# Optimization experiments

Measured on AMD Instinct MI355X. Metric: run time of the kernel, lower is better.

## Reference

```python
import jax, jax.numpy as jnp
import numpy as np

GAMMA = 0.99
LMBD = 0.95  # lambda is unused in live math: in-loop advantages are overwritten by returns - values
EPS = 0.2
T, S, H, A = 262144, 128, 1024, 16


def setup_inputs() -> dict:
    key = jax.random.key(0)
    ks = jax.random.split(key, 12)
    states = jax.random.normal(ks[0], (T, S), jnp.float32)
    actions = jax.random.normal(ks[1], (T, A), jnp.float32)
    rewards = jax.random.normal(ks[2], (T, 1), jnp.float32)
    values = jax.random.normal(ks[3], (T, 1), jnp.float32)
    masks = jax.random.randint(ks[4], (T, 1), 0, 2, jnp.int32)
    W1 = jax.random.normal(ks[5], (S, H), jnp.float32) / np.sqrt(S)
    b1 = jnp.zeros((H,), jnp.float32)
    W_mu = jax.random.normal(ks[6], (H, A), jnp.float32) / np.sqrt(H)
    b_mu = jnp.zeros((A,), jnp.float32)
    W_lv = jax.random.normal(ks[7], (H, A), jnp.float32) / np.sqrt(H)
    b_lv = jnp.zeros((A,), jnp.float32)
    # beta (old policy) log-probs: computed from the same net + small noise so that
    # ratio = exp(sum(pi_logp - beta_logp)) stays numerically reasonable, as in real PPO.
    h = jnp.tanh(states @ W1 + b1)
    mu = h @ W_mu + b_mu
    std = jnp.exp(0.5 * (h @ W_lv + b_lv))
    logp = -0.5 * jnp.square((actions - mu) / std) - jnp.log(std) - 0.5 * jnp.log(2.0 * jnp.pi)
    beta_log_probs = logp + 0.01 * jax.random.normal(ks[8], (T, A), jnp.float32)
    return dict(states=states, actions=actions, rewards=rewards, values=values,
                beta_log_probs=beta_log_probs, W1=W1, b1=b1, W_mu=W_mu, b_mu=b_mu,
                W_lv=W_lv, b_lv=b_lv, masks=masks)


def reference(states, actions, rewards, values, beta_log_probs,
              W1, b1, W_mu, b_mu, W_lv, b_lv, masks):
    m = masks.astype(rewards.dtype)  # [T,1] 1=continue, 0=episode boundary

    # reversed masked discounted-return recurrence: returns[i] = r[i] + gamma * prev_return * m[i]
    def step(prev_ret, inp):
        r, mi = inp
        ret = r + GAMMA * prev_ret * mi
        return ret, ret

    _, returns = jax.lax.scan(step, jnp.zeros((1,), rewards.dtype), (rewards, m), reverse=True)
    # (deltas / in-loop GAE advantages in the source are dead code: overwritten below)
    advantages = returns - values                      # [T,1]
    a_hat = (advantages - advantages.mean()) / (advantages.std(ddof=1) + 1e-7)

    # pi(states) -> mu, logvar (value head unused here)
    h = jnp.tanh(states @ W1 + b1)                     # [T,H]
    mu = h @ W_mu + b_mu                               # [T,A]
    logvar = h @ W_lv + b_lv
    std = jnp.exp(0.5 * logvar)
    pi_log_probs = -0.5 * jnp.square((actions - mu) / std) - jnp.log(std) - 0.5 * jnp.log(2.0 * jnp.pi)

    blp = jax.lax.stop_gradient(beta_log_probs)        # .detach() in source
    ratio = jnp.exp(jnp.sum(pi_log_probs - blp, axis=1, keepdims=True))  # [T,1]

    actor_loss = -jnp.mean(jnp.minimum(ratio * a_hat,
                                       jnp.clip(ratio, 1.0 - EPS, 1.0 + EPS) * a_hat))
    critic_loss = jnp.mean(jnp.square(advantages))
    return actor_loss + critic_loss
```

## Files before the change

### kernel.cpp

```cpp
#include <hip/hip_runtime.h>
#include <math.h>


typedef __attribute__((ext_vector_type(8))) short short8_t;
typedef __attribute__((ext_vector_type(4))) short short4_t;
typedef __attribute__((ext_vector_type(4))) float float4_t;
typedef __attribute__((ext_vector_type(2))) unsigned uint2_t;
typedef __attribute__((ext_vector_type(4))) unsigned uint4_t;

#define T_TOTAL 262144
#define S_DIM 128
#define H_DIM 1024
#define A_DIM 16
#define GAMMA 0.99f
#define LOG2E2 2.8853900817779268f
#define SEG_LEN 64
#define NSEG 4096
#define GRP 16
#define NGRP 256

#define WS_SUM   0
#define WS_SUMSQ 1
#define WS_TERM  4
#define WS_SEGA  8
#define WS_SEGB  (WS_SEGA + NSEG)
#define WS_INC   (WS_SEGB + NSEG)
#define WS_ADV   (WS_INC + NSEG)
#define WS_W1F   (WS_ADV + T_TOTAL)
#define WS_WHF   (WS_W1F + 65536)
#define WS_B1S   (WS_WHF + 16384)

#define SM_SIZE 16400

__device__ __forceinline__ short f2bf(float f) {
  unsigned u = __float_as_uint(f);
  u += 0x7fffu + ((u >> 16) & 1u);
  return (short)(u >> 16);
}

__device__ __forceinline__ unsigned cvt_pk_bf16(float lo, float hi) {
  unsigned r;
  asm("v_cvt_pk_bf16_f32 %0, %1, %2" : "=v"(r) : "v"(lo), "v"(hi));
  return r;
}

__device__ __forceinline__ void permlane32_swap2(unsigned& a, unsigned& b) {
  asm("v_permlane32_swap_b32 %0, %1" : "+v"(a), "+v"(b));
}

__device__ __forceinline__ float tanh2(float x, float bs) {
  float a = __builtin_fmaf(x, LOG2E2, bs);
  float e = __builtin_amdgcn_exp2f(a);
  float r = __builtin_amdgcn_rcpf(e + 1.0f);
  return __builtin_fmaf(r, -2.0f, 1.0f);
}

__global__ void prep_all(const float* __restrict__ W1,
                         const float* __restrict__ W_mu,
                         const float* __restrict__ W_lv,
                         const float* __restrict__ b1,
                         const float* __restrict__ rewards,
                         const int* __restrict__ masks,
                         float* __restrict__ ws,
                         short* __restrict__ w1f,
                         short* __restrict__ whf) {
  const int blk = blockIdx.x;
  if (blk < 64) {
    int id = blk * 256 + threadIdx.x;
    int lane = id & 63;
    int kf = (id >> 6) & 3;
    int nt = id >> 8;
    int quad = lane >> 4, col = nt * 16 + (lane & 15);
    int kbase = kf * 32 + quad * 8;
#pragma unroll
    for (int e = 0; e < 8; ++e)
      w1f[(size_t)id * 8 + e] = f2bf(W1[(size_t)(kbase + e) * H_DIM + col]);
  } else if (blk < 80) {
    int id = (blk - 64) * 256 + threadIdx.x;
    int lane = id & 63;
    int kf = (id >> 6) & 31;
    int nt = id >> 11;
    const float* src = nt ? W_lv : W_mu;
    int quad = lane >> 4, col = lane & 15;
    int hbase = kf * 32 + ((quad >> 1) << 4) + ((quad & 1) << 2);
#pragma unroll
    for (int e = 0; e < 8; ++e) {
      int hh = hbase + ((e >> 2) << 3) + (e & 3);
      whf[(size_t)id * 8 + e] = f2bf(src[(size_t)hh * A_DIM + col]);
    }
  } else if (blk < 96) {
    int g = (blk - 80) * 256 + threadIdx.x;
    int lo = g * SEG_LEN;
    const float4* r4 = (const float4*)(rewards + lo);
    const int4* m4 = (const int4*)(masks + lo);
    float a = 1.0f, b = 0.0f;
#pragma unroll 4
    for (int c = 15; c >= 0; --c) {
      float4 r = r4[c]; int4 mm = m4[c];
      float gi;
      gi = GAMMA * (float)mm.w; b = r.w + gi * b; a = gi * a;
      gi = GAMMA * (float)mm.z; b = r.z + gi * b; a = gi * a;
      gi = GAMMA * (float)mm.y; b = r.y + gi * b; a = gi * a;
      gi = GAMMA * (float)mm.x; b = r.x + gi * b; a = gi * a;
    }
    ws[WS_SEGA + g] = a;
    ws[WS_SEGB + g] = b;
  } else {
    if (threadIdx.x < 8) ws[threadIdx.x] = 0.0f;
    int base = threadIdx.x * 4;
    float4 bv = *(const float4*)(b1 + base);
    float4 o;
    o.x = LOG2E2 * bv.x; o.y = LOG2E2 * bv.y;
    o.z = LOG2E2 * bv.z; o.w = LOG2E2 * bv.w;
    *(float4*)(ws + WS_B1S + base) = o;
  }
}

__global__ void scan_pass2(float* __restrict__ ws) {
  __shared__ float gA[NGRP], gB[NGRP], ginc[NGRP];
  int t = threadIdx.x;
  int lo = t * GRP, hi = lo + GRP - 1;
  float A = 1.0f, B = 0.0f;
  for (int s = hi; s >= lo; --s) {
    float as = ws[WS_SEGA + s], bs = ws[WS_SEGB + s];
    B = bs + as * B;
    A = as * A;
  }
  gA[t] = A; gB[t] = B;
  __syncthreads();
  if (t == 0) {
    float x = 0.0f;
    ginc[NGRP - 1] = 0.0f;
    for (int g = NGRP - 1; g >= 1; --g) {
      x = gB[g] + gA[g] * x;
      ginc[g - 1] = x;
    }
  }
  __syncthreads();
  float x = ginc[t];
  for (int s = hi; s >= lo; --s) {
    ws[WS_INC + s] = x;
    x = ws[WS_SEGB + s] + ws[WS_SEGA + s] * x;
  }
}

__global__ void scan_pass3(const float* __restrict__ rewards,
                           const int* __restrict__ masks,
                           const float* __restrict__ values,
                           float* __restrict__ ws) {
  int g = blockIdx.x * blockDim.x + threadIdx.x;
  int lo = g * SEG_LEN;
  float x = ws[WS_INC + g];
  const float4* r4 = (const float4*)(rewards + lo);
  const int4* m4 = (const int4*)(masks + lo);
  const float4* v4 = (const float4*)(values + lo);
  float4* adv4 = (float4*)(ws + WS_ADV + lo);
  float s1 = 0.0f, s2 = 0.0f;
#pragma unroll 4
  for (int c = 15; c >= 0; --c) {
    float4 r = r4[c]; int4 mm = m4[c]; float4 v = v4[c];
    float gi;
    gi = GAMMA * (float)mm.w; x = r.w + gi * x; float aw = x - v.w;
    gi = GAMMA * (float)mm.z; x = r.z + gi * x; float az = x - v.z;
    gi = GAMMA * (float)mm.y; x = r.y + gi * x; float ay = x - v.y;
    gi = GAMMA * (float)mm.x; x = r.x + gi * x; float ax = x - v.x;
    float4 o; o.x = ax; o.y = ay; o.z = az; o.w = aw;
    adv4[c] = o;
    s1 += ax + ay + az + aw;
    s2 += ax * ax + ay * ay + az * az + aw * aw;
  }
  for (int m = 1; m < 64; m <<= 1) {
    s1 += __shfl_xor(s1, m);
    s2 += __shfl_xor(s2, m);
  }
  if ((threadIdx.x & 63) == 0) {
    atomicAdd(&ws[WS_SUM], s1);
    atomicAdd(&ws[WS_SUMSQ], s2);
  }
}

__launch_bounds__(256, 2)
__global__ void main2(const float* __restrict__ states,
                      const float* __restrict__ actions,
                      const float* __restrict__ beta,
                      const float* __restrict__ b1s,
                      const float* __restrict__ bmug,
                      const float* __restrict__ blvg,
                      const short* __restrict__ W1f,
                      const short* __restrict__ Whf,
                      float* __restrict__ ws) {
  __shared__ __align__(16) unsigned char smem[SM_SIZE];
  short* Ab = (short*)smem;

  const int tid = threadIdx.x;
  const int lane = tid & 63;
  const int w = tid >> 6;
  const int quad = lane >> 4;
  const int t0 = blockIdx.x * 64;

  {
    const float4* src = (const float4*)(states + (size_t)t0 * S_DIM);
#pragma unroll
    for (int i = 0; i < 8; ++i) {
      int f = tid + i * 256;
      float4 v = src[f];
      int row = f >> 5, kq = f & 31;
      int rt = row >> 4, rr = row & 15;
      int k = kq * 4, kf = k >> 5, qd = (k >> 3) & 3, j0 = k & 7;
      uint2_t pk2;
      pk2[0] = cvt_pk_bf16(v.x, v.y);
      pk2[1] = cvt_pk_bf16(v.z, v.w);
      *(uint2_t*)(Ab + (((rt * 4 + kf) * 64 + qd * 16 + rr) << 3) + j0) = pk2;
    }
  }
  __syncthreads();

  short8_t sfrag[4][4];
#pragma unroll
  for (int rt = 0; rt < 4; ++rt)
#pragma unroll
    for (int kf = 0; kf < 4; ++kf)
      sfrag[rt][kf] = *((const short8_t*)Ab + (rt * 4 + kf) * 64 + lane);

  float4_t acc2[4][2];
#pragma unroll
  for (int rt = 0; rt < 4; ++rt) {
    acc2[rt][0] = (float4_t){0.f, 0.f, 0.f, 0.f};
    acc2[rt][1] = (float4_t){0.f, 0.f, 0.f, 0.f};
  }
  const float4_t zz = (float4_t){0.f, 0.f, 0.f, 0.f};

  for (int kk = 0; kk < 8; ++kk) {
    const int nt1 = w * 16 + kk * 2;
    const short8_t* w1p = (const short8_t*)W1f + nt1 * 256 + lane;
    short8_t wf0[4], wf1[4];
#pragma unroll
    for (int kf = 0; kf < 4; ++kf) {
      wf0[kf] = w1p[kf * 64];
      wf1[kf] = w1p[256 + kf * 64];
    }
    const float4 b1a = *(const float4*)(b1s + nt1 * 16 + quad * 4);
    const float4 b1b = *(const float4*)(b1s + nt1 * 16 + 16 + quad * 4);
    const int kf2 = w * 8 + kk;
    const short8_t* whp = (const short8_t*)Whf + kf2 * 64 + lane;
    const short8_t wmu = whp[0];
    const short8_t wlv = whp[2048];
#pragma unroll
    for (int rt = 0; rt < 4; ++rt) {
      float4_t c0 = zz;
      float4_t c1 = zz;
#pragma unroll
      for (int kf = 0; kf < 4; ++kf) {
        c0 = __builtin_amdgcn_mfma_f32_16x16x32_bf16(wf0[kf], sfrag[rt][kf], c0, 0, 0, 0);
        c1 = __builtin_amdgcn_mfma_f32_16x16x32_bf16(wf1[kf], sfrag[rt][kf], c1, 0, 0, 0);
      }
      unsigned p00 = cvt_pk_bf16(tanh2(c0[0], b1a.x), tanh2(c0[1], b1a.y));
      unsigned p01 = cvt_pk_bf16(tanh2(c0[2], b1a.z), tanh2(c0[3], b1a.w));
      unsigned p10 = cvt_pk_bf16(tanh2(c1[0], b1b.x), tanh2(c1[1], b1b.y));
      unsigned p11 = cvt_pk_bf16(tanh2(c1[2], b1b.z), tanh2(c1[3], b1b.w));
      permlane32_swap2(p00, p10);
      permlane32_swap2(p01, p11);
      uint4_t u = (uint4_t){p00, p01, p10, p11};
      short8_t b2 = __builtin_bit_cast(short8_t, u);
      acc2[rt][0] = __builtin_amdgcn_mfma_f32_16x16x32_bf16(wmu, b2, acc2[rt][0], 0, 0, 0);
      acc2[rt][1] = __builtin_amdgcn_mfma_f32_16x16x32_bf16(wlv, b2, acc2[rt][1], 0, 0, 0);
    }
  }

  __syncthreads();
  float* red = (float*)smem;
  float* lds_term = (float*)(smem + 16384);
  if (w < 2) {
#pragma unroll
    for (int rt = 0; rt < 4; ++rt)
#pragma unroll
      for (int nt = 0; nt < 2; ++nt)
        *(float4_t*)(red + ((((w & 1) * 8 + rt * 2 + nt) * 64 + lane) << 2)) = acc2[rt][nt];
  }
  __syncthreads();
  if (w >= 2) {
#pragma unroll
    for (int rt = 0; rt < 4; ++rt)
#pragma unroll
      for (int nt = 0; nt < 2; ++nt) {
        float* p = red + ((((w & 1) * 8 + rt * 2 + nt) * 64 + lane) << 2);
        float4_t v = *(float4_t*)p;
        v += acc2[rt][nt];
        *(float4_t*)p = v;
      }
  }
  __syncthreads();

  const float s1 = ws[WS_SUM], s2 = ws[WS_SUMSQ];
  const float n = (float)T_TOTAL;
  const float mean = s1 / n;
  float var = (s2 - s1 * s1 / n) / (n - 1.0f);
  var = fmaxf(var, 0.0f);
  const float istd = 1.0f / (sqrtf(var) + 1e-7f);

  const int rt = w;
  const int tcol = lane & 15;
  const int t = t0 + rt * 16 + tcol;
  const float4 bmu4 = *(const float4*)(bmug + quad * 4);
  const float4 blv4 = *(const float4*)(blvg + quad * 4);
  float m0 = bmu4.x, m1 = bmu4.y, m2 = bmu4.z, m3 = bmu4.w;
  float l0 = blv4.x, l1 = blv4.y, l2 = blv4.z, l3 = blv4.w;
  const float4_t* rp = (const float4_t*)red;
#pragma unroll
  for (int r = 0; r < 2; ++r) {
    float4_t mv = rp[(r * 8 + rt * 2 + 0) * 64 + lane];
    float4_t lvv = rp[(r * 8 + rt * 2 + 1) * 64 + lane];
    m0 += mv[0]; m1 += mv[1]; m2 += mv[2]; m3 += mv[3];
    l0 += lvv[0]; l1 += lvv[1]; l2 += lvv[2]; l3 += lvv[3];
  }
  const float4 av = *(const float4*)(actions + (size_t)t * A_DIM + quad * 4);
  const float4 bv = *(const float4*)(beta + (size_t)t * A_DIM + quad * 4);
  float d = 0.0f;
  {
    float isd, z;
    isd = __expf(-0.5f * l0); z = (av.x - m0) * isd;
    d += -0.5f * z * z - 0.5f * l0 - 0.9189385332046727f - bv.x;
    isd = __expf(-0.5f * l1); z = (av.y - m1) * isd;
    d += -0.5f * z * z - 0.5f * l1 - 0.9189385332046727f - bv.y;
    isd = __expf(-0.5f * l2); z = (av.z - m2) * isd;
    d += -0.5f * z * z - 0.5f * l2 - 0.9189385332046727f - bv.z;
    isd = __expf(-0.5f * l3); z = (av.w - m3) * isd;
    d += -0.5f * z * z - 0.5f * l3 - 0.9189385332046727f - bv.w;
  }
  d += __shfl_xor(d, 16);
  d += __shfl_xor(d, 32);
  float term = 0.0f;
  if (quad == 0) {
    float ratio = __expf(d);
    float ah = (ws[WS_ADV + t] - mean) * istd;
    float rc = fminf(fmaxf(ratio, 0.8f), 1.2f);
    term = fminf(ratio * ah, rc * ah);
  }
  term += __shfl_xor(term, 1);
  term += __shfl_xor(term, 2);
  term += __shfl_xor(term, 4);
  term += __shfl_xor(term, 8);
  if (lane == 0) lds_term[w] = term;
  __syncthreads();
  if (tid == 0)
    atomicAdd(&ws[WS_TERM], lds_term[0] + lds_term[1] + lds_term[2] + lds_term[3]);
}

__global__ void finalize(const float* __restrict__ ws, float* __restrict__ out) {
  if (threadIdx.x == 0) {
    float n = (float)T_TOTAL;
    out[0] = ws[WS_SUMSQ] / n - ws[WS_TERM] / n;
  }
}

extern "C" void kernel_launch(void* const* d_in, const int* in_sizes, int n_in,
                              void* d_out, int out_size, void* d_ws, size_t ws_size,
                              hipStream_t stream) {
  const float* states  = (const float*)d_in[0];
  const float* actions = (const float*)d_in[1];
  const float* rewards = (const float*)d_in[2];
  const float* values  = (const float*)d_in[3];
  const float* beta    = (const float*)d_in[4];
  const float* W1      = (const float*)d_in[5];
  const float* b1      = (const float*)d_in[6];
  const float* W_mu    = (const float*)d_in[7];
  const float* b_mu    = (const float*)d_in[8];
  const float* W_lv    = (const float*)d_in[9];
  const float* b_lv    = (const float*)d_in[10];
  const int*   masks   = (const int*)d_in[11];
  float* ws = (float*)d_ws;
  float* out = (float*)d_out;
  short* w1f = (short*)(ws + WS_W1F);
  short* whf = (short*)(ws + WS_WHF);
  const float* b1s = ws + WS_B1S;

  hipLaunchKernelGGL(prep_all, dim3(97), dim3(256), 0, stream,
                     W1, W_mu, W_lv, b1, rewards, masks, ws, w1f, whf);
  hipLaunchKernelGGL(scan_pass2, dim3(1), dim3(NGRP), 0, stream, ws);
  hipLaunchKernelGGL(scan_pass3, dim3(NSEG / 256), dim3(256), 0, stream,
                     rewards, masks, values, ws);
  hipLaunchKernelGGL(main2, dim3(T_TOTAL / 64), dim3(256), 0, stream,
                     states, actions, beta, b1s, b_mu, b_lv, w1f, whf, ws);
  hipLaunchKernelGGL(finalize, dim3(1), dim3(64), 0, stream, ws, out);
}
```

Baseline: 326.9 us.

## Fold advantage statistics into segment scan and recompute returns inside main kernel

Drops the third scan pass. Each segment now also stores affine partial sums, so the second pass can form the global mean and std of the advantages analytically from segment carry-ins. The main kernel rebuilds each block's returns with an in-wave parallel scan seeded by the segment carry-in, so the advantage array no longer goes to global memory and back. It also stops keeping all state fragments in registers, loading them per row tile instead, and raises the launch bound to four blocks per SIMD to gain occupancy. The cost is more reloads of W1 fragments and slightly different floating-point rounding of the sums.

Result: slower. 421.9 us (+29.0%).

```diff
diff --git a/kernel.cpp b/kernel.cpp
--- a/kernel.cpp
+++ b/kernel.cpp
@@ -21,16 +21,22 @@
 
 #define WS_SUM   0
 #define WS_SUMSQ 1
+#define WS_MEAN  2
+#define WS_ISTD  3
 #define WS_TERM  4
 #define WS_SEGA  8
 #define WS_SEGB  (WS_SEGA + NSEG)
 #define WS_INC   (WS_SEGB + NSEG)
-#define WS_ADV   (WS_INC + NSEG)
-#define WS_W1F   (WS_ADV + T_TOTAL)
+#define WS_SEGP  (WS_INC + NSEG)
+#define WS_SEGQ  (WS_SEGP + NSEG)
+#define WS_SEGR  (WS_SEGQ + NSEG)
+#define WS_SEGS2 (WS_SEGR + NSEG)
+#define WS_SEGT2 (WS_SEGS2 + NSEG)
+#define WS_B1S   (WS_SEGT2 + NSEG)
+#define WS_W1F   (WS_B1S + 1024)
 #define WS_WHF   (WS_W1F + 65536)
-#define WS_B1S   (WS_WHF + 16384)
-
-#define SM_SIZE 16400
+
+#define SM_SIZE (16384 + 256 + 16)
 
 __device__ __forceinline__ short f2bf(float f) {
   unsigned u = __float_as_uint(f);
@@ -61,6 +67,7 @@
                          const float* __restrict__ b1,
                          const float* __restrict__ rewards,
                          const int* __restrict__ masks,
+                         const float* __restrict__ values,
                          float* __restrict__ ws,
                          short* __restrict__ w1f,
                          short* __restrict__ whf) {
@@ -93,18 +100,29 @@
     int lo = g * SEG_LEN;
     const float4* r4 = (const float4*)(rewards + lo);
     const int4* m4 = (const int4*)(masks + lo);
+    const float4* v4 = (const float4*)(values + lo);
     float a = 1.0f, b = 0.0f;
+    float P = 0.0f, Q = 0.0f, R = 0.0f, S2 = 0.0f, T2 = 0.0f;
 #pragma unroll 4
     for (int c = 15; c >= 0; --c) {
-      float4 r = r4[c]; int4 mm = m4[c];
-      float gi;
+      float4 r = r4[c]; int4 mm = m4[c]; float4 v = v4[c];
+      float gi, d;
       gi = GAMMA * (float)mm.w; b = r.w + gi * b; a = gi * a;
+      d = b - v.w; P += a; Q += d; R += a * d; S2 += d * d; T2 += a * a;
       gi = GAMMA * (float)mm.z; b = r.z + gi * b; a = gi * a;
+      d = b - v.z; P += a; Q += d; R += a * d; S2 += d * d; T2 += a * a;
       gi = GAMMA * (float)mm.y; b = r.y + gi * b; a = gi * a;
+      d = b - v.y; P += a; Q += d; R += a * d; S2 += d * d; T2 += a * a;
       gi = GAMMA * (float)mm.x; b = r.x + gi * b; a = gi * a;
+      d = b - v.x; P += a; Q += d; R += a * d; S2 += d * d; T2 += a * a;
     }
     ws[WS_SEGA + g] = a;
     ws[WS_SEGB + g] = b;
+    ws[WS_SEGP + g] = P;
+    ws[WS_SEGQ + g] = Q;
+    ws[WS_SEGR + g] = R;
+    ws[WS_SEGS2 + g] = S2;
+    ws[WS_SEGT2 + g] = T2;
   } else {
     if (threadIdx.x < 8) ws[threadIdx.x] = 0.0f;
     int base = threadIdx.x * 4;
@@ -118,6 +136,7 @@
 
 __global__ void scan_pass2(float* __restrict__ ws) {
   __shared__ float gA[NGRP], gB[NGRP], ginc[NGRP];
+  __shared__ float rs1[4], rs2[4];
   int t = threadIdx.x;
   int lo = t * GRP, hi = lo + GRP - 1;
   float A = 1.0f, B = 0.0f;
@@ -138,51 +157,44 @@
   }
   __syncthreads();
   float x = ginc[t];
+  float sum = 0.0f, sumsq = 0.0f;
   for (int s = hi; s >= lo; --s) {
     ws[WS_INC + s] = x;
+    float P = ws[WS_SEGP + s], Q = ws[WS_SEGQ + s], R = ws[WS_SEGR + s];
+    float S2 = ws[WS_SEGS2 + s], T2 = ws[WS_SEGT2 + s];
+    sum += Q + P * x;
+    sumsq += S2 + (2.0f * R + T2 * x) * x;
     x = ws[WS_SEGB + s] + ws[WS_SEGA + s] * x;
   }
-}
-
-__global__ void scan_pass3(const float* __restrict__ rewards,
-                           const int* __restrict__ masks,
-                           const float* __restrict__ values,
-                           float* __restrict__ ws) {
-  int g = blockIdx.x * blockDim.x + threadIdx.x;
-  int lo = g * SEG_LEN;
-  float x = ws[WS_INC + g];
-  const float4* r4 = (const float4*)(rewards + lo);
-  const int4* m4 = (const int4*)(masks + lo);
-  const float4* v4 = (const float4*)(values + lo);
-  float4* adv4 = (float4*)(ws + WS_ADV + lo);
-  float s1 = 0.0f, s2 = 0.0f;
-#pragma unroll 4
-  for (int c = 15; c >= 0; --c) {
-    float4 r = r4[c]; int4 mm = m4[c]; float4 v = v4[c];
-    float gi;
-    gi = GAMMA * (float)mm.w; x = r.w + gi * x; float aw = x - v.w;
-    gi = GAMMA * (float)mm.z; x = r.z + gi * x; float az = x - v.z;
-    gi = GAMMA * (float)mm.y; x = r.y + gi * x; float ay = x - v.y;
-    gi = GAMMA * (float)mm.x; x = r.x + gi * x; float ax = x - v.x;
-    float4 o; o.x = ax; o.y = ay; o.z = az; o.w = aw;
-    adv4[c] = o;
-    s1 += ax + ay + az + aw;
-    s2 += ax * ax + ay * ay + az * az + aw * aw;
-  }
+  int lane = t & 63, wv = t >> 6;
+#pragma unroll
   for (int m = 1; m < 64; m <<= 1) {
-    s1 += __shfl_xor(s1, m);
-    s2 += __shfl_xor(s2, m);
-  }
-  if ((threadIdx.x & 63) == 0) {
-    atomicAdd(&ws[WS_SUM], s1);
-    atomicAdd(&ws[WS_SUMSQ], s2);
-  }
-}
-
-__launch_bounds__(256, 2)
+    sum += __shfl_xor(sum, m);
+    sumsq += __shfl_xor(sumsq, m);
+  }
+  if (lane == 0) { rs1[wv] = sum; rs2[wv] = sumsq; }
+  __syncthreads();
+  if (t == 0) {
+    float s1 = rs1[0] + rs1[1] + rs1[2] + rs1[3];
+    float s2 = rs2[0] + rs2[1] + rs2[2] + rs2[3];
+    float n = (float)T_TOTAL;
+    ws[WS_SUM] = s1;
+    ws[WS_SUMSQ] = s2;
+    float mean = s1 / n;
+    float var = (s2 - s1 * s1 / n) / (n - 1.0f);
+    var = fmaxf(var, 0.0f);
+    ws[WS_MEAN] = mean;
+    ws[WS_ISTD] = 1.0f / (sqrtf(var) + 1e-7f);
+  }
+}
+
+__launch_bounds__(256, 4)
 __global__ void main2(const float* __restrict__ states,
                       const float* __restrict__ actions,
                       const float* __restrict__ beta,
+                      const float* __restrict__ rewards,
+                      const int* __restrict__ masks,
+                      const float* __restrict__ values,
                       const float* __restrict__ b1s,
                       const float* __restrict__ bmug,
                       const float* __restrict__ blvg,
@@ -191,12 +203,29 @@
                       float* __restrict__ ws) {
   __shared__ __align__(16) unsigned char smem[SM_SIZE];
   short* Ab = (short*)smem;
+  float* adv_lds = (float*)(smem + 16384);
+  float* lds_term = (float*)(smem + 16384 + 256);
 
   const int tid = threadIdx.x;
   const int lane = tid & 63;
   const int w = tid >> 6;
   const int quad = lane >> 4;
   const int t0 = blockIdx.x * 64;
+
+  if (w == 0) {
+    float r = rewards[t0 + lane];
+    float g = GAMMA * (float)masks[t0 + lane];
+    float v = values[t0 + lane];
+    float SA = g, SB = r;
+#pragma unroll
+    for (int off = 1; off < 64; off <<= 1) {
+      float tA = __shfl_down(SA, off);
+      float tB = __shfl_down(SB, off);
+      if (lane + off < 64) { SB = SB + SA * tB; SA = SA * tA; }
+    }
+    float x = ws[WS_INC + blockIdx.x];
+    adv_lds[lane] = (SB + SA * x) - v;
+  }
 
   {
     const float4* src = (const float4*)(states + (size_t)t0 * S_DIM);
@@ -215,13 +244,6 @@
   }
   __syncthreads();
 
-  short8_t sfrag[4][4];
-#pragma unroll
-  for (int rt = 0; rt < 4; ++rt)
-#pragma unroll
-    for (int kf = 0; kf < 4; ++kf)
-      sfrag[rt][kf] = *((const short8_t*)Ab + (rt * 4 + kf) * 64 + lane);
-
   float4_t acc2[4][2];
 #pragma unroll
   for (int rt = 0; rt < 4; ++rt) {
@@ -230,34 +252,38 @@
   }
   const float4_t zz = (float4_t){0.f, 0.f, 0.f, 0.f};
 
-  for (int kk = 0; kk < 8; ++kk) {
-    const int nt1 = w * 16 + kk * 2;
-    const short8_t* w1p = (const short8_t*)W1f + nt1 * 256 + lane;
-    short8_t wf0[4], wf1[4];
-#pragma unroll
-    for (int kf = 0; kf < 4; ++kf) {
-      wf0[kf] = w1p[kf * 64];
-      wf1[kf] = w1p[256 + kf * 64];
-    }
-    const float4 b1a = *(const float4*)(b1s + nt1 * 16 + quad * 4);
-    const float4 b1b = *(const float4*)(b1s + nt1 * 16 + 16 + quad * 4);
-    const int kf2 = w * 8 + kk;
-    const short8_t* whp = (const short8_t*)Whf + kf2 * 64 + lane;
-    const short8_t wmu = whp[0];
-    const short8_t wlv = whp[2048];
-#pragma unroll
-    for (int rt = 0; rt < 4; ++rt) {
+  for (int rt = 0; rt < 4; ++rt) {
+    short8_t sf[4];
+#pragma unroll
+    for (int kf = 0; kf < 4; ++kf)
+      sf[kf] = *((const short8_t*)Ab + (rt * 4 + kf) * 64 + lane);
+
+    for (int kk = 0; kk < 8; ++kk) {
+      const int kf2 = w * 8 + kk;
+      const short8_t* whp = (const short8_t*)Whf + kf2 * 64 + lane;
+      const short8_t wmu = whp[0];
+      const short8_t wlv = whp[2048];
+      const int nt0 = w * 16 + kk * 2;
+      const short8_t* w1p = (const short8_t*)W1f + nt0 * 256 + lane;
+
       float4_t c0 = zz;
-      float4_t c1 = zz;
-#pragma unroll
-      for (int kf = 0; kf < 4; ++kf) {
-        c0 = __builtin_amdgcn_mfma_f32_16x16x32_bf16(wf0[kf], sfrag[rt][kf], c0, 0, 0, 0);
-        c1 = __builtin_amdgcn_mfma_f32_16x16x32_bf16(wf1[kf], sfrag[rt][kf], c1, 0, 0, 0);
-      }
+      c0 = __builtin_amdgcn_mfma_f32_16x16x32_bf16(w1p[0],   sf[0], c0, 0, 0, 0);
+      c0 = __builtin_amdgcn_mfma_f32_16x16x32_bf16(w1p[64],  sf[1], c0, 0, 0, 0);
+      c0 = __builtin_amdgcn_mfma_f32_16x16x32_bf16(w1p[128], sf[2], c0, 0, 0, 0);
+      c0 = __builtin_amdgcn_mfma_f32_16x16x32_bf16(w1p[192], sf[3], c0, 0, 0, 0);
+      const float4 b1a = *(const float4*)(b1s + nt0 * 16 + quad * 4);
       unsigned p00 = cvt_pk_bf16(tanh2(c0[0], b1a.x), tanh2(c0[1], b1a.y));
       unsigned p01 = cvt_pk_bf16(tanh2(c0[2], b1a.z), tanh2(c0[3], b1a.w));
+
+      float4_t c1 = zz;
+      c1 = __builtin_amdgcn_mfma_f32_16x16x32_bf16(w1p[256], sf[0], c1, 0, 0, 0);
+      c1 = __builtin_amdgcn_mfma_f32_16x16x32_bf16(w1p[320], sf[1], c1, 0, 0, 0);
+      c1 = __builtin_amdgcn_mfma_f32_16x16x32_bf16(w1p[384], sf[2], c1, 0, 0, 0);
+      c1 = __builtin_amdgcn_mfma_f32_16x16x32_bf16(w1p[448], sf[3], c1, 0, 0, 0);
+      const float4 b1b = *(const float4*)(b1s + nt0 * 16 + 16 + quad * 4);
       unsigned p10 = cvt_pk_bf16(tanh2(c1[0], b1b.x), tanh2(c1[1], b1b.y));
       unsigned p11 = cvt_pk_bf16(tanh2(c1[2], b1b.z), tanh2(c1[3], b1b.w));
+
       permlane32_swap2(p00, p10);
       permlane32_swap2(p01, p11);
       uint4_t u = (uint4_t){p00, p01, p10, p11};
@@ -269,7 +295,6 @@
 
   __syncthreads();
   float* red = (float*)smem;
-  float* lds_term = (float*)(smem + 16384);
   if (w < 2) {
 #pragma unroll
     for (int rt = 0; rt < 4; ++rt)
@@ -291,12 +316,7 @@
   }
   __syncthreads();
 
-  const float s1 = ws[WS_SUM], s2 = ws[WS_SUMSQ];
-  const float n = (float)T_TOTAL;
-  const float mean = s1 / n;
-  float var = (s2 - s1 * s1 / n) / (n - 1.0f);
-  var = fmaxf(var, 0.0f);
-  const float istd = 1.0f / (sqrtf(var) + 1e-7f);
+  const float mean = ws[WS_MEAN], istd = ws[WS_ISTD];
 
   const int rt = w;
   const int tcol = lane & 15;
@@ -332,7 +352,7 @@
   float term = 0.0f;
   if (quad == 0) {
     float ratio = __expf(d);
-    float ah = (ws[WS_ADV + t] - mean) * istd;
+    float ah = (adv_lds[rt * 16 + tcol] - mean) * istd;
     float rc = fminf(fmaxf(ratio, 0.8f), 1.2f);
     term = fminf(ratio * ah, rc * ah);
   }
@@ -375,11 +395,10 @@
   const float* b1s = ws + WS_B1S;
 
   hipLaunchKernelGGL(prep_all, dim3(97), dim3(256), 0, stream,
-                     W1, W_mu, W_lv, b1, rewards, masks, ws, w1f, whf);
+                     W1, W_mu, W_lv, b1, rewards, masks, values, ws, w1f, whf);
   hipLaunchKernelGGL(scan_pass2, dim3(1), dim3(NGRP), 0, stream, ws);
-  hipLaunchKernelGGL(scan_pass3, dim3(NSEG / 256), dim3(256), 0, stream,
-                     rewards, masks, values, ws);
   hipLaunchKernelGGL(main2, dim3(T_TOTAL / 64), dim3(256), 0, stream,
-                     states, actions, beta, b1s, b_mu, b_lv, w1f, whf, ws);
+                     states, actions, beta, rewards, masks, values,
+                     b1s, b_mu, b_lv, w1f, whf, ws);
   hipLaunchKernelGGL(finalize, dim3(1), dim3(64), 0, stream, ws, out);
 }
```
